# Optimization experiments

Hardware: AMD Instinct MI355X
Metric: run time of the kernel (lower is better)

## Reference

```python
import jax, jax.numpy as jnp
import numpy as np

H, W = 192, 640  # image feature-map size (x_rgb[0].shape[2:])


def _pts2img(coor, feat):
    """coor: [N,2] normalized (u,v) in [0,1]; feat: [N,C] -> [C,H,W].
    Mirrors pts2img: swap to (v,u), scale by (H,W), truncate to int,
    last-write-wins scatter into (H+1,W+1,C), crop the overflow row/col."""
    coor = jnp.clip(coor, 0.0, 1.0)
    rc = (coor[:, ::-1] * jnp.array([H, W], coor.dtype)).astype(jnp.int32)  # [N,2] (row,col)
    grid = jnp.zeros((H + 1, W + 1, feat.shape[1]), feat.dtype)
    grid = grid.at[rc[:, 0], rc[:, 1]].set(feat)
    return grid[:H, :W].transpose(2, 0, 1)  # [C,H,W]


def _conv1x1(x, Wm, b):
    # x: [B,C,H,W], Wm: [O,C]
    return jnp.einsum('bchw,oc->bohw', x, Wm) + b[None, :, None, None]


def _conv3x3(x, Wk, b):
    y = jax.lax.conv_general_dilated(x, Wk, window_strides=(1, 1),
                                     padding=((1, 1), (1, 1)),
                                     dimension_numbers=('NCHW', 'OIHW', 'NCHW'))
    return y + b[None, :, None, None]


def setup_inputs() -> dict:
    key = jax.random.key(0)
    ks = jax.random.split(key, 16)
    B, C_IMG = 2, 64
    N0, C0 = 40000, 32
    N1, C1 = 20000, 64
    CL = C1 + 3  # 67
    s = 0.05
    return {
        'x_rgb0': jax.random.normal(ks[0], (B, C_IMG, H, W), jnp.float32),
        'feat0': jax.random.normal(ks[1], (B, N0, C0), jnp.float32),
        'coor0': jax.random.uniform(ks[2], (B, N0, 2), jnp.float32),
        'vox0': jax.random.normal(ks[3], (B, N0, 3), jnp.float32),
        'feat1': jax.random.normal(ks[4], (B, N1, C1), jnp.float32),
        'coor1': jax.random.uniform(ks[5], (B, N1, 2), jnp.float32),
        'vox1': jax.random.normal(ks[6], (B, N1, 3), jnp.float32),
        'W_red0': s * jax.random.normal(ks[7], (CL, C0 + 3), jnp.float32),
        'b_red0': s * jax.random.normal(ks[8], (CL,), jnp.float32),
        'W_red2': s * jax.random.normal(ks[9], (CL, CL), jnp.float32),
        'b_red2': s * jax.random.normal(ks[10], (CL,), jnp.float32),
        'W_red3': s * jax.random.normal(ks[11], (1, C_IMG), jnp.float32),
        'b_red3': s * jax.random.normal(ks[12], (1,), jnp.float32),
        'W_sp': s * jax.random.normal(ks[13], (1, CL, 3, 3), jnp.float32),
        'b_sp': s * jax.random.normal(ks[14], (1,), jnp.float32),
    }


def reference(x_rgb0, feat0, coor0, vox0, feat1, coor1, vox1,
              W_red0, b_red0, W_red2, b_red2, W_red3, b_red3, W_sp, b_sp):
    scatter = jax.vmap(_pts2img)  # over batch
    # level features = cat(sparse features, 3D voxel coords)
    pts_img0 = scatter(coor0, jnp.concatenate([feat0, vox0], axis=-1))  # [B,35,H,W]
    pts_img1 = scatter(coor1, jnp.concatenate([feat1, vox1], axis=-1))  # [B,67,H,W]
    # voxel_idx = [0,1]: 1x1 reduce on level 0, residual add of level 1
    enhanced = _conv1x1(pts_img0, W_red0, b_red0) + pts_img1
    enhanced = _conv1x1(enhanced, W_red2, b_red2)
    gated = _conv1x1(x_rgb0, W_red3, b_red3)  # [B,1,H,W], broadcasts over 67 ch
    fused = gated + enhanced
    att = jax.nn.sigmoid(_conv3x3(fused, W_sp, b_sp))  # [B,1,H,W]
    return x_rgb0 * att
```

## Files before the change

kernel.cpp:

```cpp
#include <hip/hip_runtime.h>

namespace {
constexpr int kH = 192, kW = 640, kHW = kH * kW;
constexpr int kW4g = kW / 4;
constexpr int kHW4 = kHW / 4;
constexpr int kB = 2, kC = 64;
constexpr int kN0 = 40000, kC0 = 32;
constexpr int kN1 = 20000, kC1 = 64;
constexpr int kCL = 67;
constexpr int kBHW = kB * kHW;
constexpr int kWin4 = 2 * kBHW / 4;
constexpr int kScatB = 469;
constexpr int kGateB0 = 470;
constexpr int kGateB = kB * kHW4 / 64;
constexpr int kTH2 = 8, kTW2 = 32;
constexpr int kTilesX2 = kW / kTW2;
constexpr int kTilesY2 = kH / kTH2;
constexpr int kTilesPB = kTilesX2 * kTilesY2;
constexpr int kHaloH2 = kTH2 + 2, kHaloW2 = kTW2 + 2;
constexpr int kHaloN2 = kHaloH2 * kHaloW2;

typedef float vf4 __attribute__((ext_vector_type(4)));

__global__ __launch_bounds__(256) void kinit(int4* __restrict__ win4) {
  int i = blockIdx.x * 256 + threadIdx.x;
  if (i < kWin4) win4[i] = make_int4(-1, -1, -1, -1);
}

__global__ __launch_bounds__(256) void k2(
    const float* __restrict__ coor0, const float* __restrict__ coor1,
    int* __restrict__ win0, int* __restrict__ win1,
    const float* __restrict__ W0, const float* __restrict__ b0,
    const float* __restrict__ W2, const float* __restrict__ b2,
    const float* __restrict__ Wsp, float* __restrict__ M0,
    float* __restrict__ A1g, float* __restrict__ sb, float* __restrict__ wsum,
    const float* __restrict__ x_rgb, const float* __restrict__ W3,
    float* __restrict__ g) {
  __shared__ float W2s[kCL * kCL];
  __shared__ float W0s[kCL * 35];
  __shared__ float Wsps[kCL * 9];
  __shared__ float A1s[9 * kCL];
  __shared__ float bps[kCL];
  const int bid = blockIdx.x;
  const int t = threadIdx.x;
  if (bid >= kGateB0) {
    __shared__ float4 part[4][64];
    const int gg = t & 63, q = t >> 6;
    const int gran = (bid - kGateB0) * 64 + gg;
    const int b = gran / kHW4;
    const int p4 = gran - b * kHW4;
    const float4* xr = (const float4*)(x_rgb + (size_t)b * kC * kHW) + p4;
    float4 acc = make_float4(0.f, 0.f, 0.f, 0.f);
#pragma unroll
    for (int cc = 0; cc < 16; ++cc) {
      const int c = q * 16 + cc;
      float wv = W3[c];
      float4 x4 = xr[(size_t)c * kHW4];
      acc.x += wv * x4.x;
      acc.y += wv * x4.y;
      acc.z += wv * x4.z;
      acc.w += wv * x4.w;
    }
    part[q][gg] = acc;
    __syncthreads();
    if (t < 64) {
      float4 p0 = part[0][t], p1 = part[1][t], p2 = part[2][t],
             p3 = part[3][t];
      float4 s;
      s.x = p0.x + p1.x + p2.x + p3.x;
      s.y = p0.y + p1.y + p2.y + p3.y;
      s.z = p0.z + p1.z + p2.z + p3.z;
      s.w = p0.w + p1.w + p2.w + p3.w;
      ((float4*)g)[(bid - kGateB0) * 64 + t] = s;
    }
    return;
  }
  if (bid < kScatB) {
    int idx = bid * 256 + t;
    const float* coor;
    int* win;
    int N;
    if (idx < kB * kN0) {
      coor = coor0; win = win0; N = kN0;
    } else {
      idx -= kB * kN0;
      if (idx >= kB * kN1) return;
      coor = coor1; win = win1; N = kN1;
    }
    int b = idx / N;
    float u = coor[(size_t)idx * 2 + 0];
    float v = coor[(size_t)idx * 2 + 1];
    u = fminf(fmaxf(u, 0.f), 1.f);
    v = fminf(fmaxf(v, 0.f), 1.f);
    int r = (int)(v * (float)kH);
    int c = (int)(u * (float)kW);
    if (r < kH && c < kW) {
      int n = idx - b * N;
      atomicMax(&win[b * kHW + r * kW + c], n);
    }
    return;
  }
  for (int i = t; i < kCL * kCL; i += 256) W2s[i] = W2[i];
  for (int i = t; i < kCL * 35; i += 256) W0s[i] = W0[i];
  for (int i = t; i < kCL * 9; i += 256) Wsps[i] = Wsp[i];
  __syncthreads();
  if (t < kCL) {
    float s = b2[t];
    for (int j = 0; j < kCL; ++j) s += W2s[t * kCL + j] * b0[j];
    bps[t] = s;
  }
  for (int idx = t; idx < 9 * kCL; idx += 256) {
    int k = idx / kCL, j = idx - k * kCL;
    float s = 0.f;
    for (int c = 0; c < kCL; ++c) s += Wsps[c * 9 + k] * W2s[c * kCL + j];
    A1s[idx] = s;
    A1g[idx] = s;
  }
  __syncthreads();
  for (int idx = t; idx < 9 * 35; idx += 256) {
    int k = idx / 35, i = idx - k * 35;
    float s = 0.f;
    for (int j = 0; j < kCL; ++j) s += A1s[k * kCL + j] * W0s[j * 35 + i];
    M0[idx] = s;
  }
  if (t < 9) {
    float s = 0.f;
    for (int c = 0; c < kCL; ++c) s += Wsps[c * 9 + t] * bps[c];
    sb[t] = s;
  } else if (t >= 16 && t < 25) {
    int k = t - 16;
    float s = 0.f;
    for (int c = 0; c < kCL; ++c) s += Wsps[c * 9 + k];
    wsum[k] = s;
  }
}

__global__ __launch_bounds__(256) void kgym(
    const float* __restrict__ x_rgb, const float* __restrict__ g,
    const int* __restrict__ win0, const int* __restrict__ win1,
    const float* __restrict__ feat0, const float* __restrict__ vox0,
    const float* __restrict__ feat1, const float* __restrict__ vox1,
    const float* __restrict__ M0, const float* __restrict__ A1,
    const float* __restrict__ sb, const float* __restrict__ wsum,
    const float* __restrict__ b3, const float* __restrict__ bsp,
    float* __restrict__ out) {
  __shared__ float ylds[9][kHaloH2][kHaloW2];
  __shared__ float att[256 + 8];
  const int t = threadIdx.x;
  const int tile = blockIdx.x;
  const int b = tile / kTilesPB;
  const int tr = tile - b * kTilesPB;
  const int ty = tr / kTilesX2, tx = tr - ty * kTilesX2;
  const int h0 = ty * kTH2, w0 = tx * kTW2;

  for (int i = t; i < kHaloN2; i += 256) {
    const int hh = i / kHaloW2, ww = i - hh * kHaloW2;
    const int h = h0 + hh - 1, w = w0 + ww - 1;
    float y[9];
    if (h < 0 || h >= kH || w < 0 || w >= kW) {
#pragma unroll
      for (int k = 0; k < 9; ++k) y[k] = 0.f;
    } else {
      const int pix = b * kHW + h * kW + w;
      const float gv = b3[0] + g[pix];
#pragma unroll
      for (int k = 0; k < 9; ++k) y[k] = wsum[k] * gv + sb[k];
      const int w0i = win0[pix];
      if (w0i >= 0) {
        const float4* f0 =
            (const float4*)(feat0 + ((size_t)b * kN0 + w0i) * kC0);
#pragma unroll
        for (int i4 = 0; i4 < 8; ++i4) {
          float4 v = f0[i4];
#pragma unroll
          for (int k = 0; k < 9; ++k) {
            const float* m = M0 + k * 35 + i4 * 4;
            y[k] += m[0] * v.x + m[1] * v.y + m[2] * v.z + m[3] * v.w;
          }
        }
        const float* v0 = vox0 + ((size_t)b * kN0 + w0i) * 3;
#pragma unroll
        for (int ii = 0; ii < 3; ++ii) {
          float v = v0[ii];
#pragma unroll
          for (int k = 0; k < 9; ++k) y[k] += M0[k * 35 + kC0 + ii] * v;
        }
      }
      const int w1i = win1[pix];
      if (w1i >= 0) {
        const float4* f1 =
            (const float4*)(feat1 + ((size_t)b * kN1 + w1i) * kC1);
#pragma unroll
        for (int i4 = 0; i4 < 16; ++i4) {
          float4 v = f1[i4];
#pragma unroll
          for (int k = 0; k < 9; ++k) {
            const float* m = A1 + k * kCL + i4 * 4;
            y[k] += m[0] * v.x + m[1] * v.y + m[2] * v.z + m[3] * v.w;
          }
        }
        const float* v1 = vox1 + ((size_t)b * kN1 + w1i) * 3;
#pragma unroll
        for (int ii = 0; ii < 3; ++ii) {
          float v = v1[ii];
#pragma unroll
          for (int k = 0; k < 9; ++k) y[k] += A1[k * kCL + kC1 + ii] * v;
        }
      }
    }
#pragma unroll
    for (int k = 0; k < 9; ++k) ylds[k][hh][ww] = y[k];
  }
  __syncthreads();

  {
    const int lh = t >> 5, lw = t & 31;
    float logit = bsp[0];
#pragma unroll
    for (int r = 0; r < 3; ++r) {
#pragma unroll
      for (int d = 0; d < 3; ++d) logit += ylds[3 * r + d][lh + r][lw + d];
    }
    att[t] = 1.f / (1.f + __expf(-logit));
  }
  __syncthreads();

  const int gi = t & 63, cg = t >> 6;
  const int gr = gi >> 3, gc = gi & 7;
  const int gran = (h0 + gr) * kW4g + tx * 8 + gc;
  const float4 a4 = *(const float4*)&att[gr * 32 + gc * 4];
  const vf4* xr = (const vf4*)(x_rgb + (size_t)b * kC * kHW) + gran;
  vf4* op = (vf4*)(out + (size_t)b * kC * kHW) + gran;
#pragma unroll
  for (int cc = 0; cc < 16; ++cc) {
    const int c = cg * 16 + cc;
    vf4 x4 = __builtin_nontemporal_load(xr + (size_t)c * kHW4);
    vf4 r4;
    r4.x = x4.x * a4.x;
    r4.y = x4.y * a4.y;
    r4.z = x4.z * a4.z;
    r4.w = x4.w * a4.w;
    __builtin_nontemporal_store(r4, op + (size_t)c * kHW4);
  }
}

}

extern "C" void kernel_launch(void* const* d_in, const int* in_sizes, int n_in,
                              void* d_out, int out_size, void* d_ws,
                              size_t ws_size, hipStream_t stream) {
  const float* x_rgb = (const float*)d_in[0];
  const float* feat0 = (const float*)d_in[1];
  const float* coor0 = (const float*)d_in[2];
  const float* vox0 = (const float*)d_in[3];
  const float* feat1 = (const float*)d_in[4];
  const float* coor1 = (const float*)d_in[5];
  const float* vox1 = (const float*)d_in[6];
  const float* W0 = (const float*)d_in[7];
  const float* b0 = (const float*)d_in[8];
  const float* W2 = (const float*)d_in[9];
  const float* b2 = (const float*)d_in[10];
  const float* W3 = (const float*)d_in[11];
  const float* b3 = (const float*)d_in[12];
  const float* Wsp = (const float*)d_in[13];
  const float* bsp = (const float*)d_in[14];
  float* out = (float*)d_out;

  float* g = (float*)d_ws;
  int* win0 = (int*)(g + (size_t)kBHW);
  int* win1 = win0 + (size_t)kBHW;
  float* M0 = (float*)(win1 + (size_t)kBHW);
  float* A1 = M0 + 9 * 35;
  float* sb = A1 + 9 * kCL;
  float* wsum = sb + 9;

  kinit<<<(kWin4 + 255) / 256, 256, 0, stream>>>((int4*)win0);
  k2<<<kGateB0 + kGateB, 256, 0, stream>>>(coor0, coor1, win0, win1, W0, b0,
                                           W2, b2, Wsp, M0, A1, sb, wsum,
                                           x_rgb, W3, g);
  kgym<<<kB * kTilesPB, 256, 0, stream>>>(x_rgb, g, win0, win1, feat0, vox0,
                                          feat1, vox1, M0, A1, sb, wsum, b3,
                                          bsp, out);
}
```

Baseline: 76.83 us.

## Split fused attention+multiply kernel into separate attention and broadcast-multiply kernels

New measurement: 91.14 us. +18.6%, slower.

```diff
diff --git a/kernel.cpp b/kernel.cpp
--- a/kernel.cpp
+++ b/kernel.cpp
@@ -2,7 +2,6 @@
 
 namespace {
 constexpr int kH = 192, kW = 640, kHW = kH * kW;
-constexpr int kW4g = kW / 4;
 constexpr int kHW4 = kHW / 4;
 constexpr int kB = 2, kC = 64;
 constexpr int kN0 = 40000, kC0 = 32;
@@ -13,12 +12,12 @@
 constexpr int kScatB = 469;
 constexpr int kGateB0 = 470;
 constexpr int kGateB = kB * kHW4 / 64;
-constexpr int kTH2 = 8, kTW2 = 32;
-constexpr int kTilesX2 = kW / kTW2;
-constexpr int kTilesY2 = kH / kTH2;
-constexpr int kTilesPB = kTilesX2 * kTilesY2;
-constexpr int kHaloH2 = kTH2 + 2, kHaloW2 = kTW2 + 2;
-constexpr int kHaloN2 = kHaloH2 * kHaloW2;
+constexpr int kTH = 8, kTW = 16;
+constexpr int kTilesX = kW / kTW;
+constexpr int kTilesY = kH / kTH;
+constexpr int kTilesPB = kTilesX * kTilesY;
+constexpr int kHaloH = kTH + 2, kHaloW = kTW + 2;
+constexpr int kHaloN = kHaloH * kHaloW;
 
 typedef float vf4 __attribute__((ext_vector_type(4)));
 
@@ -135,26 +134,24 @@
   }
 }
 
-__global__ __launch_bounds__(256) void kgym(
-    const float* __restrict__ x_rgb, const float* __restrict__ g,
-    const int* __restrict__ win0, const int* __restrict__ win1,
-    const float* __restrict__ feat0, const float* __restrict__ vox0,
-    const float* __restrict__ feat1, const float* __restrict__ vox1,
-    const float* __restrict__ M0, const float* __restrict__ A1,
-    const float* __restrict__ sb, const float* __restrict__ wsum,
-    const float* __restrict__ b3, const float* __restrict__ bsp,
-    float* __restrict__ out) {
-  __shared__ float ylds[9][kHaloH2][kHaloW2];
-  __shared__ float att[256 + 8];
+__global__ __launch_bounds__(256) void katt(
+    const float* __restrict__ g, const int* __restrict__ win0,
+    const int* __restrict__ win1, const float* __restrict__ feat0,
+    const float* __restrict__ vox0, const float* __restrict__ feat1,
+    const float* __restrict__ vox1, const float* __restrict__ M0,
+    const float* __restrict__ A1, const float* __restrict__ sb,
+    const float* __restrict__ wsum, const float* __restrict__ b3,
+    const float* __restrict__ bsp, float* __restrict__ att) {
+  __shared__ float ylds[9][kHaloH][kHaloW];
   const int t = threadIdx.x;
   const int tile = blockIdx.x;
   const int b = tile / kTilesPB;
   const int tr = tile - b * kTilesPB;
-  const int ty = tr / kTilesX2, tx = tr - ty * kTilesX2;
-  const int h0 = ty * kTH2, w0 = tx * kTW2;
-
-  for (int i = t; i < kHaloN2; i += 256) {
-    const int hh = i / kHaloW2, ww = i - hh * kHaloW2;
+  const int ty = tr / kTilesX, tx = tr - ty * kTilesX;
+  const int h0 = ty * kTH, w0 = tx * kTW;
+
+  if (t < kHaloN) {
+    const int hh = t / kHaloW, ww = t - hh * kHaloW;
     const int h = h0 + hh - 1, w = w0 + ww - 1;
     float y[9];
     if (h < 0 || h >= kH || w < 0 || w >= kW) {
@@ -213,35 +210,34 @@
   }
   __syncthreads();
 
-  {
-    const int lh = t >> 5, lw = t & 31;
+  if (t < kTH * kTW) {
+    const int lh = t / kTW, lw = t - lh * kTW;
     float logit = bsp[0];
 #pragma unroll
     for (int r = 0; r < 3; ++r) {
 #pragma unroll
       for (int d = 0; d < 3; ++d) logit += ylds[3 * r + d][lh + r][lw + d];
     }
-    att[t] = 1.f / (1.f + __expf(-logit));
-  }
-  __syncthreads();
-
-  const int gi = t & 63, cg = t >> 6;
-  const int gr = gi >> 3, gc = gi & 7;
-  const int gran = (h0 + gr) * kW4g + tx * 8 + gc;
-  const float4 a4 = *(const float4*)&att[gr * 32 + gc * 4];
-  const vf4* xr = (const vf4*)(x_rgb + (size_t)b * kC * kHW) + gran;
-  vf4* op = (vf4*)(out + (size_t)b * kC * kHW) + gran;
-#pragma unroll
-  for (int cc = 0; cc < 16; ++cc) {
-    const int c = cg * 16 + cc;
-    vf4 x4 = __builtin_nontemporal_load(xr + (size_t)c * kHW4);
-    vf4 r4;
-    r4.x = x4.x * a4.x;
-    r4.y = x4.y * a4.y;
-    r4.z = x4.z * a4.z;
-    r4.w = x4.w * a4.w;
-    __builtin_nontemporal_store(r4, op + (size_t)c * kHW4);
-  }
+    att[b * kHW + (h0 + lh) * kW + (w0 + lw)] =
+        1.f / (1.f + __expf(-logit));
+  }
+}
+
+__global__ __launch_bounds__(256) void kmul(const float* __restrict__ x_rgb,
+                                            const float* __restrict__ att,
+                                            float* __restrict__ out) {
+  const int i = blockIdx.x * 256 + threadIdx.x;
+  const int b = i / (kC * kHW4);
+  const int r = i - b * (kC * kHW4);
+  const int p4 = r % kHW4;
+  float4 a4 = ((const float4*)att)[b * kHW4 + p4];
+  vf4 x4 = __builtin_nontemporal_load((const vf4*)x_rgb + i);
+  vf4 r4;
+  r4.x = x4.x * a4.x;
+  r4.y = x4.y * a4.y;
+  r4.z = x4.z * a4.z;
+  r4.w = x4.w * a4.w;
+  __builtin_nontemporal_store(r4, (vf4*)out + i);
 }
 
 }
@@ -267,7 +263,8 @@
   float* out = (float*)d_out;
 
   float* g = (float*)d_ws;
-  int* win0 = (int*)(g + (size_t)kBHW);
+  float* att = g + (size_t)kBHW;
+  int* win0 = (int*)(att + (size_t)kBHW);
   int* win1 = win0 + (size_t)kBHW;
   float* M0 = (float*)(win1 + (size_t)kBHW);
   float* A1 = M0 + 9 * 35;
@@ -278,7 +275,8 @@
   k2<<<kGateB0 + kGateB, 256, 0, stream>>>(coor0, coor1, win0, win1, W0, b0,
                                            W2, b2, Wsp, M0, A1, sb, wsum,
                                            x_rgb, W3, g);
-  kgym<<<kB * kTilesPB, 256, 0, stream>>>(x_rgb, g, win0, win1, feat0, vox0,
-                                          feat1, vox1, M0, A1, sb, wsum, b3,
-                                          bsp, out);
-}
+  katt<<<kB * kTilesPB, 256, 0, stream>>>(g, win0, win1, feat0, vox0, feat1,
+                                          vox1, M0, A1, sb, wsum, b3, bsp,
+                                          att);
+  kmul<<<kB * kC * kHW4 / 256, 256, 0, stream>>>(x_rgb, att, out);
+}
```
